# Kernel tuning notes

Hardware: AMD Instinct MI355X
Metric: run time of the kernel (lower is better)

The kernel has to match this reference:

```python
import jax, jax.numpy as jnp
import numpy as np

B, S, D = 4, 16, 512          # batch, seq, attention_dim
V, T = 32000, 18              # vocab_size, tree_depth
INNER = V - 1                 # internal nodes of Huffman tree


def setup_inputs() -> dict:
    key = jax.random.key(0)
    k_att, k_w, k_idx, k_bit = jax.random.split(key, 4)
    att = jax.random.normal(k_att, (B, S, D), dtype=jnp.float32)
    weight = jax.random.normal(k_w, (INNER, D), dtype=jnp.float32) * 0.02
    path_index = jax.random.randint(k_idx, (V * T,), 0, INNER, dtype=jnp.int64)
    # left/right branch bits: sign=+1,bias=0 -> p ; sign=-1,bias=1 -> 1-p
    bits = jax.random.randint(k_bit, (V * T,), 0, 2).astype(jnp.float32)
    path_sign = 1.0 - 2.0 * bits
    path_bias = bits
    return {
        "att": att,
        "weight": weight,
        "path_index": path_index,
        "path_sign": path_sign,
        "path_bias": path_bias,
        "vocab_size": V,
        "tree_depth": T,
    }


def reference(att, weight, path_index, path_sign, path_bias, vocab_size, tree_depth):
    # h: sigmoid of linear projection onto internal-node vectors  [B,S,INNER]
    h = jax.nn.sigmoid(jnp.einsum("bsd,nd->bsn", att, weight))
    # gather per-(token,depth) internal-node probs, flip via sign/bias
    g = jnp.take(h, path_index, axis=-1) * path_sign + path_bias  # [B,S,V*T]
    Hm = g.reshape(att.shape[0], -1, vocab_size, tree_depth)      # [B,S,V,T]
    return jnp.sum(jnp.log(Hm), axis=-1)                          # [B,S,V]
```

## Files before the change

kernel.cpp:

```cpp
#include <hip/hip_runtime.h>
#include <hip/hip_bf16.h>

#define BS    64
#define DDIM  512
#define NV    32000
#define TD    18
#define INNER 31999
#define ROWX  32000

#define CFG_IDX_I64   8u

typedef __attribute__((ext_vector_type(8))) short short8;
typedef __attribute__((ext_vector_type(4))) float floatx4;

__device__ __forceinline__ float bf16_to_f32(unsigned short u) {
    union { unsigned int i; float f; } v; v.i = ((unsigned int)u) << 16; return v.f;
}
__device__ __forceinline__ unsigned short f32_to_bf16(float f) {
    union { float f; unsigned int i; } v; v.f = f;
    unsigned int r = v.i + 0x7FFFu + ((v.i >> 16) & 1u);
    return (unsigned short)(r >> 16);
}

__global__ void probe_idx(const unsigned int* __restrict__ idx_w,
                          unsigned int* __restrict__ cfg)
{
    if (threadIdx.x == 0) {
        bool i64 = true;
        for (int i = 1; i < 16; i += 2) i64 &= (idx_w[i] == 0u);
        *cfg = i64 ? CFG_IDX_I64 : 0u;
    }
}

__global__ __launch_bounds__(256) void cvt_att(
    const float4* __restrict__ att, ushort4* __restrict__ attb)
{
    int i = blockIdx.x * 256 + threadIdx.x;
    float4 a = att[i];
    ushort4 r;
    r.x = f32_to_bf16(a.x); r.y = f32_to_bf16(a.y);
    r.z = f32_to_bf16(a.z); r.w = f32_to_bf16(a.w);
    attb[i] = r;
}

__global__ __launch_bounds__(256) void prep_idx2(
    const int* __restrict__ idx,
    const unsigned int* __restrict__ signbits,
    unsigned short* __restrict__ idx2,
    const unsigned int* __restrict__ cfgp)
{
    const unsigned int cfg = *cfgp;
    int i = blockIdx.x * 256 + threadIdx.x;
    int v = (cfg & CFG_IDX_I64) ? idx[2 * i] : idx[i];
    idx2[i] = (unsigned short)((v << 1) | (int)(signbits[i] >> 31));
}

__global__ __launch_bounds__(256) void gemm_x(
    const unsigned short* __restrict__ attb,
    const float* __restrict__ weight,
    unsigned short* __restrict__ tabx)
{
    const int lane = threadIdx.x & 63;
    const int wave = threadIdx.x >> 6;
    const int nb   = blockIdx.x * 64 + wave * 16;
    const int l15  = lane & 15;
    const int quad = lane >> 4;

    floatx4 acc[4];
#pragma unroll
    for (int i = 0; i < 4; ++i) acc[i] = (floatx4){0.f, 0.f, 0.f, 0.f};

    int brow = nb + l15;
    if (brow > INNER - 1) brow = INNER - 1;
    const float*          bbase = weight + (size_t)brow * DDIM + quad * 8;
    const unsigned short* abase = attb + l15 * DDIM + quad * 8;

#pragma unroll 4
    for (int k0 = 0; k0 < DDIM; k0 += 32) {
        float4 b0 = *(const float4*)(bbase + k0);
        float4 b1 = *(const float4*)(bbase + k0 + 4);
        short8 bfrag;
        bfrag[0] = (short)f32_to_bf16(b0.x); bfrag[1] = (short)f32_to_bf16(b0.y);
        bfrag[2] = (short)f32_to_bf16(b0.z); bfrag[3] = (short)f32_to_bf16(b0.w);
        bfrag[4] = (short)f32_to_bf16(b1.x); bfrag[5] = (short)f32_to_bf16(b1.y);
        bfrag[6] = (short)f32_to_bf16(b1.z); bfrag[7] = (short)f32_to_bf16(b1.w);
#pragma unroll
        for (int mt = 0; mt < 4; ++mt) {
            short8 afrag = *(const short8*)(abase + mt * 16 * DDIM + k0);
            acc[mt] = __builtin_amdgcn_mfma_f32_16x16x32_bf16(afrag, bfrag, acc[mt], 0, 0, 0);
        }
    }

    const int n = nb + l15;
    if (n < INNER) {
#pragma unroll
        for (int mt = 0; mt < 4; ++mt) {
#pragma unroll
            for (int r = 0; r < 4; ++r) {
                const int m = mt * 16 + quad * 4 + r;
                tabx[m * ROWX + n] = f32_to_bf16(acc[mt][r]);
            }
        }
    }
}

__global__ __launch_bounds__(1024) void gather_logsig(
    const unsigned short* __restrict__ tabx,
    const unsigned short* __restrict__ idx2,
    float* __restrict__ out)
{
    __shared__ __align__(16) unsigned short lds[ROWX];
    const int bs    = blockIdx.y;
    const int vbase = blockIdx.x * 8000;
    const int tid   = threadIdx.x;

    const uint4* src = (const uint4*)(tabx + bs * ROWX);
    for (int i = tid; i < ROWX / 8; i += 1024) ((uint4*)lds)[i] = src[i];
    __syncthreads();

#pragma unroll
    for (int s = 0; s < 8; ++s) {
        int r = s * 1024 + tid;
        if (r < 8000) {
            const unsigned short* ip = idx2 + (size_t)(vbase + r) * TD;
            float sum = 0.f;
#pragma unroll
            for (int t = 0; t < TD; ++t) {
                unsigned int e = ip[t];
                float x = bf16_to_f32(lds[e >> 1]);
                float sp = fmaxf(-x, 0.f) + __logf(1.f + __expf(-fabsf(x)));
                sum -= sp + ((e & 1u) ? x : 0.f);
            }
            out[bs * NV + vbase + r] = sum;
        }
    }
}

extern "C" void kernel_launch(void* const* d_in, const int* in_sizes, int n_in,
                              void* d_out, int out_size, void* d_ws, size_t ws_size,
                              hipStream_t stream)
{
    const float*        att    = (const float*)d_in[0];
    const float*        weight = (const float*)d_in[1];
    const int*          pidx   = (const int*)d_in[2];
    const unsigned int* psign  = (const unsigned int*)d_in[3];
    float* out = (float*)d_out;

    char* ws = (char*)d_ws;
    unsigned short* tabx = (unsigned short*)ws;
    unsigned short* idx2 = (unsigned short*)(ws + 4096000);
    ushort4*        attb = (ushort4*)       (ws + 5248000);
    unsigned int*   cfg  = (unsigned int*)  (ws + 5313536);

    probe_idx<<<1, 64, 0, stream>>>((const unsigned int*)pidx, cfg);
    cvt_att  <<<32,   256, 0, stream>>>((const float4*)att, attb);
    prep_idx2<<<2250, 256, 0, stream>>>(pidx, psign, idx2, cfg);
    gemm_x   <<<500,  256, 0, stream>>>((const unsigned short*)attb, weight, tabx);
    gather_logsig<<<dim3(4, BS), 1024, 0, stream>>>(tabx, idx2, out);
}
```

Baseline: 155.5 us.

## Precompute log-sigmoid pairs in GEMM epilogue, transpose index table, merge prep kernels

The GEMM epilogue now computes log(sigmoid(x)) and log(1-sigmoid(x)) once per internal node and stores both as a packed bf16 pair. The gather then only does table lookups and adds, with no exp or log per path element. The path index table is transposed to depth-major so gather loads coalesce across threads. Three small prep kernels are merged into one launch. In exchange the table doubles to 128KB of LDS per block via dynamic shared memory, which may lower occupancy, and log-probabilities are rounded to bf16.

```diff
diff --git a/kernel.cpp b/kernel.cpp
--- a/kernel.cpp
+++ b/kernel.cpp
@@ -6,9 +6,7 @@
 #define NV    32000
 #define TD    18
 #define INNER 31999
-#define ROWX  32000
-
-#define CFG_IDX_I64   8u
+#define ROWP  32000
 
 typedef __attribute__((ext_vector_type(8))) short short8;
 typedef __attribute__((ext_vector_type(4))) float floatx4;
@@ -22,43 +20,39 @@
     return (unsigned short)(r >> 16);
 }
 
-__global__ void probe_idx(const unsigned int* __restrict__ idx_w,
-                          unsigned int* __restrict__ cfg)
+#define IDXB 2250
+__global__ __launch_bounds__(256) void prep(
+    const int* __restrict__ idx,
+    const unsigned int* __restrict__ signbits,
+    unsigned short* __restrict__ idx2T,
+    const float4* __restrict__ att,
+    ushort4* __restrict__ attb)
 {
-    if (threadIdx.x == 0) {
+    const int b = blockIdx.x;
+    if (b < IDXB) {
+        const unsigned int* w = (const unsigned int*)idx;
         bool i64 = true;
-        for (int i = 1; i < 16; i += 2) i64 &= (idx_w[i] == 0u);
-        *cfg = i64 ? CFG_IDX_I64 : 0u;
+#pragma unroll
+        for (int j = 1; j < 16; j += 2) i64 &= (w[j] == 0u);
+        int o = b * 256 + threadIdx.x;
+        int t = o / NV, v = o - t * NV;
+        int i = v * TD + t;
+        int val = i64 ? idx[2 * i] : idx[i];
+        idx2T[o] = (unsigned short)((val << 1) | (int)(signbits[i] >> 31));
+    } else {
+        int i = (b - IDXB) * 256 + threadIdx.x;
+        float4 a = att[i];
+        ushort4 r;
+        r.x = f32_to_bf16(a.x); r.y = f32_to_bf16(a.y);
+        r.z = f32_to_bf16(a.z); r.w = f32_to_bf16(a.w);
+        attb[i] = r;
     }
 }
 
-__global__ __launch_bounds__(256) void cvt_att(
-    const float4* __restrict__ att, ushort4* __restrict__ attb)
-{
-    int i = blockIdx.x * 256 + threadIdx.x;
-    float4 a = att[i];
-    ushort4 r;
-    r.x = f32_to_bf16(a.x); r.y = f32_to_bf16(a.y);
-    r.z = f32_to_bf16(a.z); r.w = f32_to_bf16(a.w);
-    attb[i] = r;
-}
-
-__global__ __launch_bounds__(256) void prep_idx2(
-    const int* __restrict__ idx,
-    const unsigned int* __restrict__ signbits,
-    unsigned short* __restrict__ idx2,
-    const unsigned int* __restrict__ cfgp)
-{
-    const unsigned int cfg = *cfgp;
-    int i = blockIdx.x * 256 + threadIdx.x;
-    int v = (cfg & CFG_IDX_I64) ? idx[2 * i] : idx[i];
-    idx2[i] = (unsigned short)((v << 1) | (int)(signbits[i] >> 31));
-}
-
-__global__ __launch_bounds__(256) void gemm_x(
+__global__ __launch_bounds__(256) void gemm_logsig(
     const unsigned short* __restrict__ attb,
     const float* __restrict__ weight,
-    unsigned short* __restrict__ tabx)
+    unsigned int* __restrict__ pairs)
 {
     const int lane = threadIdx.x & 63;
     const int wave = threadIdx.x >> 6;
@@ -98,38 +92,43 @@
 #pragma unroll
             for (int r = 0; r < 4; ++r) {
                 const int m = mt * 16 + quad * 4 + r;
-                tabx[m * ROWX + n] = f32_to_bf16(acc[mt][r]);
+                float x = acc[mt][r];
+                float lp = -(fmaxf(-x, 0.f) + __logf(1.f + __expf(-fabsf(x))));
+                float lm = lp - x;
+                pairs[m * ROWP + n] = (unsigned int)f32_to_bf16(lp)
+                                    | ((unsigned int)f32_to_bf16(lm) << 16);
             }
         }
     }
 }
 
-__global__ __launch_bounds__(1024) void gather_logsig(
-    const unsigned short* __restrict__ tabx,
-    const unsigned short* __restrict__ idx2,
+__global__ __launch_bounds__(1024) void gather_pairs(
+    const unsigned int* __restrict__ pairs,
+    const unsigned short* __restrict__ idx2T,
     float* __restrict__ out)
 {
-    __shared__ __align__(16) unsigned short lds[ROWX];
+    extern __shared__ unsigned int lds32[];
     const int bs    = blockIdx.y;
     const int vbase = blockIdx.x * 8000;
     const int tid   = threadIdx.x;
 
-    const uint4* src = (const uint4*)(tabx + bs * ROWX);
-    for (int i = tid; i < ROWX / 8; i += 1024) ((uint4*)lds)[i] = src[i];
+    const uint4* src = (const uint4*)(pairs + (size_t)bs * ROWP);
+    for (int i = tid; i < ROWP / 4; i += 1024) ((uint4*)lds32)[i] = src[i];
     __syncthreads();
 
 #pragma unroll
     for (int s = 0; s < 8; ++s) {
         int r = s * 1024 + tid;
         if (r < 8000) {
-            const unsigned short* ip = idx2 + (size_t)(vbase + r) * TD;
+            const unsigned short* col = idx2T + vbase + r;
             float sum = 0.f;
 #pragma unroll
             for (int t = 0; t < TD; ++t) {
-                unsigned int e = ip[t];
-                float x = bf16_to_f32(lds[e >> 1]);
-                float sp = fmaxf(-x, 0.f) + __logf(1.f + __expf(-fabsf(x)));
-                sum -= sp + ((e & 1u) ? x : 0.f);
+                unsigned int e = col[(size_t)t * NV];
+                unsigned int p = lds32[e >> 1];
+                unsigned short h = (e & 1u) ? (unsigned short)(p >> 16)
+                                            : (unsigned short)(p & 0xFFFFu);
+                sum += bf16_to_f32(h);
             }
             out[bs * NV + vbase + r] = sum;
         }
@@ -147,14 +146,14 @@
     float* out = (float*)d_out;
 
     char* ws = (char*)d_ws;
-    unsigned short* tabx = (unsigned short*)ws;
-    unsigned short* idx2 = (unsigned short*)(ws + 4096000);
-    ushort4*        attb = (ushort4*)       (ws + 5248000);
-    unsigned int*   cfg  = (unsigned int*)  (ws + 5313536);
+    unsigned int*   pairs = (unsigned int*)ws;
+    unsigned short* idx2T = (unsigned short*)(ws + 8192000);
+    ushort4*        attb  = (ushort4*)       (ws + 9344000);
 
-    probe_idx<<<1, 64, 0, stream>>>((const unsigned int*)pidx, cfg);
-    cvt_att  <<<32,   256, 0, stream>>>((const float4*)att, attb);
-    prep_idx2<<<2250, 256, 0, stream>>>(pidx, psign, idx2, cfg);
-    gemm_x   <<<500,  256, 0, stream>>>((const unsigned short*)attb, weight, tabx);
-    gather_logsig<<<dim3(4, BS), 1024, 0, stream>>>(tabx, idx2, out);
+    hipFuncSetAttribute(reinterpret_cast<const void*>(gather_pairs),
+                        hipFuncAttributeMaxDynamicSharedMemorySize, ROWP * 4);
+
+    prep<<<IDXB + 32, 256, 0, stream>>>(pidx, psign, idx2T, (const float4*)att, attb);
+    gemm_logsig<<<500, 256, 0, stream>>>((const unsigned short*)attb, weight, pairs);
+    gather_pairs<<<dim3(4, BS), 1024, ROWP * 4, stream>>>(pairs, idx2T, out);
 }
```

Result: faster. 145.0 us (-6.7%).
